# Kernel tuning notes

Hardware: AMD Instinct MI355X
Metric: run time of the kernel (lower is better)

Reference implementation:

```python
import jax, jax.numpy as jnp
import numpy as np

B, K, D = 4, 2048, 512   # batch, time window (self._K), d_model
H, Q, V = 8, 64, 64      # heads, per-head query dim, per-head value dim


def setup_inputs() -> dict:
    key = jax.random.key(0)
    ks = jax.random.split(key, 10)
    s = 0.05
    return {
        "query": jax.random.normal(ks[0], (B, K, D), jnp.float32),
        "key":   jax.random.normal(ks[1], (B, K, D), jnp.float32),
        "value": jax.random.normal(ks[2], (B, K, D), jnp.float32),
        # stacked per-head Linear params (torch Linear: y = x W^T + b -> store as [h, D, out])
        "W_q": jax.random.normal(ks[3], (H, D, Q), jnp.float32) * s,
        "b_q": jax.random.normal(ks[4], (H, Q), jnp.float32) * s,
        "W_k": jax.random.normal(ks[5], (H, D, Q), jnp.float32) * s,
        "b_k": jax.random.normal(ks[6], (H, Q), jnp.float32) * s,
        "W_v": jax.random.normal(ks[7], (H, D, V), jnp.float32) * s,
        "b_v": jax.random.normal(ks[8], (H, V), jnp.float32) * s,
        "W_o": jax.random.normal(ks[9], (H * V, D), jnp.float32) * s,
        "b_o": jnp.zeros((D,), jnp.float32),
    }


def reference(query, key, value, W_q, b_q, W_k, b_k, W_v, b_v, W_o, b_o):
    # per-head projections, batched over heads: [B, H, K, Q/V]
    q = jnp.einsum("bkd,hdq->bhkq", query, W_q) + b_q[None, :, None, :]
    k = jnp.einsum("bkd,hdq->bhkq", key,   W_k) + b_k[None, :, None, :]
    v = jnp.einsum("bkd,hdv->bhkv", value, W_v) + b_v[None, :, None, :]
    # NOTE: original divides by sqrt(self._K) (time window), NOT sqrt(d_k)
    scores = jnp.einsum("bhkq,bhlq->bhkl", q, k) / np.sqrt(K).astype(np.float32)
    # mask == 'subsequent': causal triu mask above the diagonal
    causal = jnp.triu(jnp.ones((K, K), bool), k=1)
    scores = jnp.where(causal[None, None], -jnp.inf, scores)
    attn = jax.nn.softmax(scores, axis=-1)
    heads = jnp.einsum("bhkl,bhlv->bhkv", attn, v)          # [B, H, K, V]
    concat = heads.transpose(0, 2, 1, 3).reshape(B, K, H * V)  # concat along last dim
    return concat @ W_o + b_o
```

## Files before the change

kernel.cpp:

```cpp
#include <hip/hip_runtime.h>
#include <hip/hip_bf16.h>

typedef __attribute__((ext_vector_type(8))) short bf16x8;
typedef __attribute__((ext_vector_type(4))) float f32x4;

#define SEQ 2048
#define DM  512
#define NH  8
#define DH  64
#define QSCALE 0.031879360f

__device__ __forceinline__ unsigned short f2bf(float f) {
  unsigned int u = __float_as_uint(f);
  unsigned int r = 0x7FFFu + ((u >> 16) & 1u);
  return (unsigned short)((u + r) >> 16);
}

__device__ __forceinline__ void load8f(const float* __restrict__ s,
                                       unsigned short* __restrict__ o) {
  float4 v0 = *(const float4*)s;
  float4 v1 = *(const float4*)(s + 4);
  o[0] = f2bf(v0.x); o[1] = f2bf(v0.y); o[2] = f2bf(v0.z); o[3] = f2bf(v0.w);
  o[4] = f2bf(v1.x); o[5] = f2bf(v1.y); o[6] = f2bf(v1.z); o[7] = f2bf(v1.w);
}

__global__ __launch_bounds__(256) void weight_prep(const float* __restrict__ Wq,
                                                   const float* __restrict__ Wk,
                                                   const float* __restrict__ Wv,
                                                   const float* __restrict__ Wo,
                                                   unsigned short* __restrict__ Wqt,
                                                   unsigned short* __restrict__ Wkt,
                                                   unsigned short* __restrict__ Wvt,
                                                   unsigned short* __restrict__ Wot) {
  const int which = blockIdx.x >> 6, wi = blockIdx.x & 63;
  const float* src;
  unsigned short* dst;
  int R, C, r0, c0;
  if (which < 3) {
    const float* W = (which == 0) ? Wq : (which == 1) ? Wk : Wv;
    unsigned short* D = (which == 0) ? Wqt : (which == 1) ? Wkt : Wvt;
    int h = wi >> 3;
    src = W + (size_t)h * 512 * 64;
    dst = D + (size_t)h * 64 * 512;
    R = 512; C = 64; r0 = (wi & 7) * 64; c0 = 0;
  } else {
    src = Wo; dst = Wot;
    R = 512; C = 512; r0 = (wi >> 3) * 64; c0 = (wi & 7) * 64;
  }
  __shared__ __align__(16) unsigned short T[64][72];
  const int tid = threadIdx.x;
#pragma unroll
  for (int i = 0; i < 2; ++i) {
    int c = tid + 256 * i;
    int lr = c >> 3, lc = (c & 7) * 8;
    __align__(16) unsigned short tmp[8];
    load8f(src + (size_t)(r0 + lr) * C + c0 + lc, tmp);
    *(uint4*)&T[lr][lc] = *(const uint4*)tmp;
  }
  __syncthreads();
#pragma unroll
  for (int i = 0; i < 2; ++i) {
    int c = tid + 256 * i;
    int orow = c >> 3, och = (c & 7) * 8;
    __align__(16) unsigned short tmp[8];
#pragma unroll
    for (int j = 0; j < 8; ++j) tmp[j] = T[och + j][orow];
    *(uint4*)(dst + (size_t)(c0 + orow) * R + r0 + och) = *(uint4*)tmp;
  }
}

__global__ __launch_bounds__(256, 4) void proj128(const float* __restrict__ q,
                                                  const float* __restrict__ k,
                                                  const float* __restrict__ v,
                                                  const unsigned short* __restrict__ Wqt,
                                                  const unsigned short* __restrict__ Wkt,
                                                  const unsigned short* __restrict__ Wvt,
                                                  const float* __restrict__ bq,
                                                  const float* __restrict__ bk,
                                                  const float* __restrict__ bv,
                                                  unsigned short* __restrict__ Qp,
                                                  unsigned short* __restrict__ Kp,
                                                  unsigned short* __restrict__ Vpt) {
  const int which = blockIdx.z;
  const float* X = (which == 0) ? q : (which == 1) ? k : v;
  const unsigned short* Wt = (which == 0) ? Wqt : (which == 1) ? Wkt : Wvt;
  const float* bias = (which == 0) ? bq : (which == 1) ? bk : bv;
  unsigned short* out = (which == 0) ? Qp : (which == 1) ? Kp : Vpt;
  const float ps = (which == 0) ? QSCALE : 1.0f;

  const int m0 = blockIdx.x * 128;
  const int n0 = blockIdx.y * 128;
  __shared__ __align__(16) unsigned short smem[2][128][72];
  unsigned short (*As)[72] = smem[0];
  unsigned short (*Bs)[72] = smem[1];
  const int tid  = threadIdx.x;
  const int wave = tid >> 6, lane = tid & 63;
  const int l15  = lane & 15, quad = lane >> 4;
  const int rb = (wave >> 1) * 64, cb = (wave & 1) * 64;

  f32x4 acc[4][4];
#pragma unroll
  for (int i = 0; i < 4; ++i)
#pragma unroll
    for (int f = 0; f < 4; ++f) acc[i][f] = (f32x4){0.f, 0.f, 0.f, 0.f};

  for (int k0 = 0; k0 < DM; k0 += 64) {
    __syncthreads();
#pragma unroll
    for (int i = 0; i < 4; ++i) {
      int c = tid + 256 * i;
      int lr = c >> 3, lc = (c & 7) * 8;
      __align__(16) unsigned short tmp[8];
      load8f(X + (size_t)(m0 + lr) * DM + k0 + lc, tmp);
      *(uint4*)&As[lr][lc] = *(const uint4*)tmp;
      *(uint4*)&Bs[lr][lc] = *(const uint4*)(Wt + (size_t)(n0 + lr) * DM + k0 + lc);
    }
    __syncthreads();
#pragma unroll
    for (int kc = 0; kc < 2; ++kc) {
      bf16x8 av[4], bv4[4];
#pragma unroll
      for (int i = 0; i < 4; ++i) av[i]  = *(const bf16x8*)&As[rb + 16 * i + l15][kc * 32 + quad * 8];
#pragma unroll
      for (int f = 0; f < 4; ++f) bv4[f] = *(const bf16x8*)&Bs[cb + 16 * f + l15][kc * 32 + quad * 8];
#pragma unroll
      for (int i = 0; i < 4; ++i)
#pragma unroll
        for (int f = 0; f < 4; ++f)
          acc[i][f] = __builtin_amdgcn_mfma_f32_16x16x32_bf16(av[i], bv4[f], acc[i][f], 0, 0, 0);
    }
  }

  if (which < 2) {
#pragma unroll
    for (int i = 0; i < 4; ++i)
#pragma unroll
      for (int f = 0; f < 4; ++f)
#pragma unroll
        for (int r = 0; r < 4; ++r) {
          int m = m0 + rb + 16 * i + quad * 4 + r;
          int col = n0 + cb + 16 * f + l15;
          int head = col >> 6, o = col & 63;
          int b = m >> 11, s = m & (SEQ - 1);
          float val = (acc[i][f][r] + bias[col]) * ps;
          out[(((size_t)(b * NH + head) * SEQ + s) << 6) + o] = f2bf(val);
        }
  } else {
    __syncthreads();
    unsigned short* T = &smem[0][0][0] + wave * 4608;
#pragma unroll
    for (int i = 0; i < 4; ++i)
#pragma unroll
      for (int f = 0; f < 4; ++f)
#pragma unroll
        for (int r = 0; r < 4; ++r) {
          int lrow = 16 * i + quad * 4 + r;
          int lcol = 16 * f + l15;
          int col = n0 + cb + 16 * f + l15;
          T[lcol * 72 + lrow] = f2bf(acc[i][f][r] + bias[col]);
        }
    const int mbase = m0 + rb;
    const int b = mbase >> 11, sbase = mbase & (SEQ - 1);
    const int head = (n0 + cb) >> 6;
    unsigned short* dstb = out + ((size_t)(b * NH + head) * DH) * SEQ + sbase;
#pragma unroll
    for (int j = 0; j < 8; ++j) {
      int dh = (lane >> 3) + j * 8;
      int sc = (lane & 7) * 8;
      *(uint4*)(dstb + (size_t)dh * SEQ + sc) = *(const uint4*)&T[dh * 72 + sc];
    }
  }
}

__global__ __launch_bounds__(512, 4) void attn_kernel(const unsigned short* __restrict__ Qp,
                                                      const unsigned short* __restrict__ Kp,
                                                      const unsigned short* __restrict__ Vpt,
                                                      unsigned short* __restrict__ concat) {
  const int bh = blockIdx.x;
  const int ip = blockIdx.y;
  const int b = bh >> 3, h = bh & 7;
  const int qa = ip, qb = 31 - ip;
  __shared__ __align__(16) unsigned short Ks[2][64][72], Vts[2][64][72], Ps[128][72];
  const int tid  = threadIdx.x;
  const int wave = tid >> 6, lane = tid & 63;
  const int l15  = lane & 15, quad = lane >> 4;
  const int w4   = wave & 3;
  const bool isB = wave < 4;
  const int qt   = isB ? qb : qa;
  const unsigned short* Qb = Qp  + (size_t)bh * SEQ * DH;
  const unsigned short* Kb = Kp  + (size_t)bh * SEQ * DH;
  const unsigned short* Vb = Vpt + (size_t)bh * DH * SEQ;

  bf16x8 aq[2];
#pragma unroll
  for (int kc = 0; kc < 2; ++kc)
    aq[kc] = *(const bf16x8*)(Qb + (size_t)(qt * 64 + 16 * w4 + l15) * DH + kc * 32 + quad * 8);

  float l_lane[4];
  f32x4 Of[4];
#pragma unroll
  for (int r = 0; r < 4; ++r) l_lane[r] = 0.f;
#pragma unroll
  for (int f = 0; f < 4; ++f) Of[f] = (f32x4){0.f, 0.f, 0.f, 0.f};

  const int sr = tid >> 3, sc = (tid & 7) * 8;
  uint4 kst, vst;

#define STAGE_LOAD(lt_) do {                                                   \
    kst = *(const uint4*)(Kb + (size_t)((lt_) * 64 + sr) * DH + sc);           \
    vst = *(const uint4*)(Vb + (size_t)sr * SEQ + (lt_) * 64 + sc);            \
  } while (0)

#define STAGE_WRITE(bi_) do {                                                  \
    *(uint4*)&Ks[bi_][sr][sc]  = kst;                                          \
    *(uint4*)&Vts[bi_][sr][sc] = vst;                                          \
  } while (0)

  STAGE_LOAD(0);
  STAGE_WRITE(0);
  STAGE_LOAD(1);
  __syncthreads();

#pragma unroll 1
  for (int lt = 0; lt <= qb; ++lt) {
    const int cur = lt & 1;
    if (lt < qb) STAGE_WRITE(cur ^ 1);
    if (lt + 2 <= qb) STAGE_LOAD(lt + 2);

    const bool act = isB || (lt <= qa);
    if (act) {
      const int l0 = lt * 64;
      f32x4 S[4];
#pragma unroll
      for (int f = 0; f < 4; ++f) S[f] = (f32x4){0.f, 0.f, 0.f, 0.f};
#pragma unroll
      for (int kc = 0; kc < 2; ++kc) {
#pragma unroll
        for (int f = 0; f < 4; ++f) {
          bf16x8 bk = *(const bf16x8*)&Ks[cur][16 * f + l15][kc * 32 + quad * 8];
          S[f] = __builtin_amdgcn_mfma_f32_16x16x32_bf16(aq[kc], bk, S[f], 0, 0, 0);
        }
      }
      if (lt == qt) {
        const int mrow = qt * 64 + 16 * w4 + quad * 4;
#pragma unroll
        for (int f = 0; f < 4; ++f)
#pragma unroll
          for (int r = 0; r < 4; ++r)
            if (l0 + 16 * f + l15 > mrow + r) S[f][r] = -1e30f;
      }
#pragma unroll
      for (int f = 0; f < 4; ++f)
#pragma unroll
        for (int r = 0; r < 4; ++r) {
          float p = __builtin_amdgcn_exp2f(S[f][r]);
          l_lane[r] += p;
          Ps[wave * 16 + quad * 4 + r][16 * f + l15] = f2bf(p);
        }
#pragma unroll
      for (int kc = 0; kc < 2; ++kc) {
        bf16x8 ap = *(const bf16x8*)&Ps[wave * 16 + l15][kc * 32 + quad * 8];
#pragma unroll
        for (int f = 0; f < 4; ++f) {
          bf16x8 bvv = *(const bf16x8*)&Vts[cur][16 * f + l15][kc * 32 + quad * 8];
          Of[f] = __builtin_amdgcn_mfma_f32_16x16x32_bf16(ap, bvv, Of[f], 0, 0, 0);
        }
      }
    }
    __syncthreads();
  }
#undef STAGE_LOAD
#undef STAGE_WRITE

#pragma unroll
  for (int d = 1; d < 16; d <<= 1)
#pragma unroll
    for (int r = 0; r < 4; ++r) l_lane[r] += __shfl_xor(l_lane[r], d);

#pragma unroll
  for (int f = 0; f < 4; ++f)
#pragma unroll
    for (int r = 0; r < 4; ++r) {
      const int row = qt * 64 + 16 * w4 + quad * 4 + r;
      const int col = h * DH + 16 * f + l15;
      concat[(size_t)(b * SEQ + row) * DM + col] = f2bf(Of[f][r] / l_lane[r]);
    }
}

__global__ __launch_bounds__(256) void gemm_out(const unsigned short* __restrict__ A,
                                                const unsigned short* __restrict__ Bt,
                                                const float* __restrict__ bias,
                                                float* __restrict__ out) {
  const int m0 = blockIdx.x * 64;
  const int nbase = blockIdx.y * 256;
  __shared__ __align__(16) unsigned short Bs[64][72];
  const int tid  = threadIdx.x;
  const int wave = tid >> 6, lane = tid & 63;
  const int l15  = lane & 15, quad = lane >> 4;

  bf16x8 afr[16];
  const unsigned short* arow = A + (size_t)(m0 + 16 * wave + l15) * DM;
#pragma unroll
  for (int k0i = 0; k0i < 8; ++k0i)
#pragma unroll
    for (int kc = 0; kc < 2; ++kc)
      afr[k0i * 2 + kc] = *(const bf16x8*)(arow + k0i * 64 + kc * 32 + quad * 8);

  for (int n0 = nbase; n0 < nbase + 256; n0 += 64) {
    f32x4 acc[4];
#pragma unroll
    for (int f = 0; f < 4; ++f) acc[f] = (f32x4){0.f, 0.f, 0.f, 0.f};
    for (int k0i = 0; k0i < 8; ++k0i) {
      __syncthreads();
#pragma unroll
      for (int i = 0; i < 2; ++i) {
        int c = tid + 256 * i;
        int lr = c >> 3, lc = (c & 7) * 8;
        *(uint4*)&Bs[lr][lc] = *(const uint4*)(Bt + (size_t)(n0 + lr) * DM + k0i * 64 + lc);
      }
      __syncthreads();
#pragma unroll
      for (int kc = 0; kc < 2; ++kc)
#pragma unroll
        for (int f = 0; f < 4; ++f) {
          bf16x8 bfv = *(const bf16x8*)&Bs[16 * f + l15][kc * 32 + quad * 8];
          acc[f] = __builtin_amdgcn_mfma_f32_16x16x32_bf16(afr[k0i * 2 + kc], bfv, acc[f], 0, 0, 0);
        }
    }
#pragma unroll
    for (int f = 0; f < 4; ++f)
#pragma unroll
      for (int r = 0; r < 4; ++r) {
        int row = 16 * wave + quad * 4 + r;
        int col = 16 * f + l15;
        out[(size_t)(m0 + row) * DM + n0 + col] = acc[f][r] + bias[n0 + col];
      }
  }
}

extern "C" void kernel_launch(void* const* d_in, const int* in_sizes, int n_in,
                              void* d_out, int out_size, void* d_ws, size_t ws_size,
                              hipStream_t stream) {
  const float* query = (const float*)d_in[0];
  const float* key   = (const float*)d_in[1];
  const float* value = (const float*)d_in[2];
  const float* W_q   = (const float*)d_in[3];
  const float* b_q   = (const float*)d_in[4];
  const float* W_k   = (const float*)d_in[5];
  const float* b_k   = (const float*)d_in[6];
  const float* W_v   = (const float*)d_in[7];
  const float* b_v   = (const float*)d_in[8];
  const float* W_o   = (const float*)d_in[9];
  const float* b_o   = (const float*)d_in[10];
  float* out = (float*)d_out;

  char* ws = (char*)d_ws;
  unsigned short* Wqt    = (unsigned short*)(ws + 0);
  unsigned short* Wkt    = (unsigned short*)(ws + 524288);
  unsigned short* Wvt    = (unsigned short*)(ws + 1048576);
  unsigned short* Wot    = (unsigned short*)(ws + 1572864);
  unsigned short* Qp     = (unsigned short*)(ws + 2097152);
  unsigned short* Kp     = (unsigned short*)(ws + 10485760);
  unsigned short* Vpt    = (unsigned short*)(ws + 18874368);
  unsigned short* concat = (unsigned short*)(ws + 27262976);

  weight_prep<<<dim3(256), 256, 0, stream>>>(W_q, W_k, W_v, W_o, Wqt, Wkt, Wvt, Wot);

  proj128<<<dim3(64, 4, 3), 256, 0, stream>>>(query, key, value, Wqt, Wkt, Wvt,
                                              b_q, b_k, b_v, Qp, Kp, Vpt);

  attn_kernel<<<dim3(32, 16), 512, 0, stream>>>(Qp, Kp, Vpt, concat);

  gemm_out<<<dim3(128, 2), 256, 0, stream>>>(concat, Wot, b_o, out);
}
```

Measured before the change: 205.2 us.

## Double-buffer LDS tiles with register prefetch in projection and output GEMMs

The projection GEMM now loads the next k-tile from global memory into registers while the current shared-memory tile feeds MFMAs, using two LDS buffers and one barrier per iteration. The output GEMM gets the same double-buffered prefetch, and its grid is split into 128-column blocks so it launches twice as many workgroups. The attention P tile row stride is padded from 72 to 76 to change the LDS bank mapping. The costs are more shared memory and registers per block, with lower occupancy bounds on both GEMMs.

After: 206.8 us. No clear change (+0.8%).

```diff
diff --git a/kernel.cpp b/kernel.cpp
--- a/kernel.cpp
+++ b/kernel.cpp
@@ -16,12 +16,17 @@
   return (unsigned short)((u + r) >> 16);
 }
 
+__device__ __forceinline__ void cvt8f(const float4& v0, const float4& v1,
+                                      unsigned short* __restrict__ o) {
+  o[0] = f2bf(v0.x); o[1] = f2bf(v0.y); o[2] = f2bf(v0.z); o[3] = f2bf(v0.w);
+  o[4] = f2bf(v1.x); o[5] = f2bf(v1.y); o[6] = f2bf(v1.z); o[7] = f2bf(v1.w);
+}
+
 __device__ __forceinline__ void load8f(const float* __restrict__ s,
                                        unsigned short* __restrict__ o) {
   float4 v0 = *(const float4*)s;
   float4 v1 = *(const float4*)(s + 4);
-  o[0] = f2bf(v0.x); o[1] = f2bf(v0.y); o[2] = f2bf(v0.z); o[3] = f2bf(v0.w);
-  o[4] = f2bf(v1.x); o[5] = f2bf(v1.y); o[6] = f2bf(v1.z); o[7] = f2bf(v1.w);
+  cvt8f(v0, v1, o);
 }
 
 __global__ __launch_bounds__(256) void weight_prep(const float* __restrict__ Wq,
@@ -69,7 +74,7 @@
   }
 }
 
-__global__ __launch_bounds__(256, 4) void proj128(const float* __restrict__ q,
+__global__ __launch_bounds__(256, 2) void proj128(const float* __restrict__ q,
                                                   const float* __restrict__ k,
                                                   const float* __restrict__ v,
                                                   const unsigned short* __restrict__ Wqt,
@@ -90,9 +95,7 @@
 
   const int m0 = blockIdx.x * 128;
   const int n0 = blockIdx.y * 128;
-  __shared__ __align__(16) unsigned short smem[2][128][72];
-  unsigned short (*As)[72] = smem[0];
-  unsigned short (*Bs)[72] = smem[1];
+  __shared__ __align__(16) unsigned short As[2][128][72], Bs[2][128][72];
   const int tid  = threadIdx.x;
   const int wave = tid >> 6, lane = tid & 63;
   const int l15  = lane & 15, quad = lane >> 4;
@@ -104,32 +107,58 @@
 #pragma unroll
     for (int f = 0; f < 4; ++f) acc[i][f] = (f32x4){0.f, 0.f, 0.f, 0.f};
 
-  for (int k0 = 0; k0 < DM; k0 += 64) {
-    __syncthreads();
-#pragma unroll
-    for (int i = 0; i < 4; ++i) {
-      int c = tid + 256 * i;
-      int lr = c >> 3, lc = (c & 7) * 8;
-      __align__(16) unsigned short tmp[8];
-      load8f(X + (size_t)(m0 + lr) * DM + k0 + lc, tmp);
-      *(uint4*)&As[lr][lc] = *(const uint4*)tmp;
-      *(uint4*)&Bs[lr][lc] = *(const uint4*)(Wt + (size_t)(n0 + lr) * DM + k0 + lc);
-    }
-    __syncthreads();
+  float4 af[4][2];
+  uint4 bst[4];
+
+#define P_LOAD(k0_) do {                                                        \
+    _Pragma("unroll")                                                           \
+    for (int i_ = 0; i_ < 4; ++i_) {                                            \
+      int c_ = tid + 256 * i_;                                                  \
+      int lr_ = c_ >> 3, lc_ = (c_ & 7) * 8;                                    \
+      const float* xp_ = X + (size_t)(m0 + lr_) * DM + (k0_) + lc_;             \
+      af[i_][0] = *(const float4*)xp_;                                          \
+      af[i_][1] = *(const float4*)(xp_ + 4);                                    \
+      bst[i_] = *(const uint4*)(Wt + (size_t)(n0 + lr_) * DM + (k0_) + lc_);    \
+    } } while (0)
+
+#define P_WRITE(bi_) do {                                                       \
+    _Pragma("unroll")                                                           \
+    for (int i_ = 0; i_ < 4; ++i_) {                                            \
+      int c_ = tid + 256 * i_;                                                  \
+      int lr_ = c_ >> 3, lc_ = (c_ & 7) * 8;                                    \
+      __align__(16) unsigned short t_[8];                                       \
+      cvt8f(af[i_][0], af[i_][1], t_);                                          \
+      *(uint4*)&As[bi_][lr_][lc_] = *(const uint4*)t_;                          \
+      *(uint4*)&Bs[bi_][lr_][lc_] = bst[i_];                                    \
+    } } while (0)
+
+  P_LOAD(0);
+  P_WRITE(0);
+  P_LOAD(64);
+  __syncthreads();
+
+#pragma unroll 1
+  for (int k0i = 0; k0i < 8; ++k0i) {
+    const int cur = k0i & 1;
+    if (k0i < 7) P_WRITE(cur ^ 1);
+    if (k0i < 6) P_LOAD((k0i + 2) * 64);
 #pragma unroll
     for (int kc = 0; kc < 2; ++kc) {
       bf16x8 av[4], bv4[4];
 #pragma unroll
-      for (int i = 0; i < 4; ++i) av[i]  = *(const bf16x8*)&As[rb + 16 * i + l15][kc * 32 + quad * 8];
-#pragma unroll
-      for (int f = 0; f < 4; ++f) bv4[f] = *(const bf16x8*)&Bs[cb + 16 * f + l15][kc * 32 + quad * 8];
+      for (int i = 0; i < 4; ++i) av[i]  = *(const bf16x8*)&As[cur][rb + 16 * i + l15][kc * 32 + quad * 8];
+#pragma unroll
+      for (int f = 0; f < 4; ++f) bv4[f] = *(const bf16x8*)&Bs[cur][cb + 16 * f + l15][kc * 32 + quad * 8];
 #pragma unroll
       for (int i = 0; i < 4; ++i)
 #pragma unroll
         for (int f = 0; f < 4; ++f)
           acc[i][f] = __builtin_amdgcn_mfma_f32_16x16x32_bf16(av[i], bv4[f], acc[i][f], 0, 0, 0);
     }
-  }
+    __syncthreads();
+  }
+#undef P_LOAD
+#undef P_WRITE
 
   if (which < 2) {
 #pragma unroll
@@ -147,7 +176,7 @@
         }
   } else {
     __syncthreads();
-    unsigned short* T = &smem[0][0][0] + wave * 4608;
+    unsigned short* T = &As[0][0][0] + wave * 4608;
 #pragma unroll
     for (int i = 0; i < 4; ++i)
 #pragma unroll
@@ -180,7 +209,7 @@
   const int ip = blockIdx.y;
   const int b = bh >> 3, h = bh & 7;
   const int qa = ip, qb = 31 - ip;
-  __shared__ __align__(16) unsigned short Ks[2][64][72], Vts[2][64][72], Ps[128][72];
+  __shared__ __align__(16) unsigned short Ks[2][64][72], Vts[2][64][72], Ps[128][76];
   const int tid  = threadIdx.x;
   const int wave = tid >> 6, lane = tid & 63;
   const int l15  = lane & 15, quad = lane >> 4;
@@ -287,13 +316,13 @@
     }
 }
 
-__global__ __launch_bounds__(256) void gemm_out(const unsigned short* __restrict__ A,
-                                                const unsigned short* __restrict__ Bt,
-                                                const float* __restrict__ bias,
-                                                float* __restrict__ out) {
+__global__ __launch_bounds__(256, 2) void gemm_out(const unsigned short* __restrict__ A,
+                                                   const unsigned short* __restrict__ Bt,
+                                                   const float* __restrict__ bias,
+                                                   float* __restrict__ out) {
   const int m0 = blockIdx.x * 64;
-  const int nbase = blockIdx.y * 256;
-  __shared__ __align__(16) unsigned short Bs[64][72];
+  const int nbase = blockIdx.y * 128;
+  __shared__ __align__(16) unsigned short Bs[2][64][72];
   const int tid  = threadIdx.x;
   const int wave = tid >> 6, lane = tid & 63;
   const int l15  = lane & 15, quad = lane >> 4;
@@ -306,36 +335,59 @@
     for (int kc = 0; kc < 2; ++kc)
       afr[k0i * 2 + kc] = *(const bf16x8*)(arow + k0i * 64 + kc * 32 + quad * 8);
 
-  for (int n0 = nbase; n0 < nbase + 256; n0 += 64) {
-    f32x4 acc[4];
-#pragma unroll
-    for (int f = 0; f < 4; ++f) acc[f] = (f32x4){0.f, 0.f, 0.f, 0.f};
-    for (int k0i = 0; k0i < 8; ++k0i) {
-      __syncthreads();
-#pragma unroll
-      for (int i = 0; i < 2; ++i) {
-        int c = tid + 256 * i;
-        int lr = c >> 3, lc = (c & 7) * 8;
-        *(uint4*)&Bs[lr][lc] = *(const uint4*)(Bt + (size_t)(n0 + lr) * DM + k0i * 64 + lc);
+  uint4 bst0, bst1;
+  const int br = tid >> 3, bc = (tid & 7) * 8;
+
+#define G_LOAD(s_) do {                                                          \
+    const int n0_ = nbase + ((s_) >> 3) * 64, k0_ = ((s_) & 7) * 64;             \
+    bst0 = *(const uint4*)(Bt + (size_t)(n0_ + br) * DM + k0_ + bc);             \
+    bst1 = *(const uint4*)(Bt + (size_t)(n0_ + br + 32) * DM + k0_ + bc);        \
+  } while (0)
+
+#define G_WRITE(bi_) do {                                                        \
+    *(uint4*)&Bs[bi_][br][bc]      = bst0;                                       \
+    *(uint4*)&Bs[bi_][br + 32][bc] = bst1;                                       \
+  } while (0)
+
+  f32x4 acc[2][4];
+#pragma unroll
+  for (int nh = 0; nh < 2; ++nh)
+#pragma unroll
+    for (int f = 0; f < 4; ++f) acc[nh][f] = (f32x4){0.f, 0.f, 0.f, 0.f};
+
+  G_LOAD(0);
+  G_WRITE(0);
+  G_LOAD(1);
+  __syncthreads();
+
+#pragma unroll
+  for (int s = 0; s < 16; ++s) {
+    const int cur = s & 1;
+    if (s < 15) G_WRITE(cur ^ 1);
+    if (s < 14) G_LOAD(s + 2);
+    const int nh = s >> 3, k0i = s & 7;
+#pragma unroll
+    for (int kc = 0; kc < 2; ++kc)
+#pragma unroll
+      for (int f = 0; f < 4; ++f) {
+        bf16x8 bfv = *(const bf16x8*)&Bs[cur][16 * f + l15][kc * 32 + quad * 8];
+        acc[nh][f] = __builtin_amdgcn_mfma_f32_16x16x32_bf16(afr[k0i * 2 + kc], bfv, acc[nh][f], 0, 0, 0);
       }
-      __syncthreads();
-#pragma unroll
-      for (int kc = 0; kc < 2; ++kc)
-#pragma unroll
-        for (int f = 0; f < 4; ++f) {
-          bf16x8 bfv = *(const bf16x8*)&Bs[16 * f + l15][kc * 32 + quad * 8];
-          acc[f] = __builtin_amdgcn_mfma_f32_16x16x32_bf16(afr[k0i * 2 + kc], bfv, acc[f], 0, 0, 0);
-        }
-    }
+    __syncthreads();
+  }
+#undef G_LOAD
+#undef G_WRITE
+
+#pragma unroll
+  for (int nh = 0; nh < 2; ++nh)
 #pragma unroll
     for (int f = 0; f < 4; ++f)
 #pragma unroll
       for (int r = 0; r < 4; ++r) {
         int row = 16 * wave + quad * 4 + r;
-        int col = 16 * f + l15;
-        out[(size_t)(m0 + row) * DM + n0 + col] = acc[f][r] + bias[n0 + col];
+        int col = nbase + nh * 64 + 16 * f + l15;
+        out[(size_t)(m0 + row) * DM + col] = acc[nh][f][r] + bias[col];
       }
-  }
 }
 
 extern "C" void kernel_launch(void* const* d_in, const int* in_sizes, int n_in,
@@ -371,5 +423,5 @@
 
   attn_kernel<<<dim3(32, 16), 512, 0, stream>>>(Qp, Kp, Vpt, concat);
 
-  gemm_out<<<dim3(128, 2), 256, 0, stream>>>(concat, Wot, b_o, out);
-}
+  gemm_out<<<dim3(128, 4), 256, 0, stream>>>(concat, Wot, b_o, out);
+}
```
